# Kernel optimization log

Measured on AMD Instinct MI355X. Metric: run time of the kernel, lower is better.

## Reference

```python
import jax, jax.numpy as jnp
import numpy as np

B, N, M, Wlen = 4, 20000, 64, 8


def setup_inputs() -> dict:
    key = jax.random.key(0)
    k1, k2, k3, k4 = jax.random.split(key, 4)
    a0 = jax.random.uniform(k1, (B, N), dtype=jnp.float32)
    W = 0.01 * jax.random.normal(k2, (M, M), dtype=jnp.float32)
    X1 = jax.random.randint(k3, (M, N, Wlen, 2), 0, N, dtype=jnp.int64)
    X2 = jax.random.randint(k4, (M, N, Wlen, 2), 0, N, dtype=jnp.int64)
    return {"a0": a0, "W": W, "X1": X1, "X2": X2, "T": 2}


def f_clause_stack(a, X):
    # a: [B,n], X: [m,n,w,2] -> [B,m,n]
    y1 = a[:, X[..., 0]]  # [B,m,n,w] gather
    y2 = a[:, X[..., 1]]
    return jnp.max(y1 * y2, axis=3)


def predicate_forward(a, W, X1, X2, temperature=1.0):
    F1 = f_clause_stack(a, X1)  # [B,m1,n]
    F2 = f_clause_stack(a, X2)  # [B,m2,n]
    pi = jax.nn.softmax((W / temperature).reshape(-1)).reshape(W.shape)  # [m1,m2]
    pi1 = pi.sum(axis=1)  # [m1]
    pi2 = pi.sum(axis=0)  # [m2]
    Eu = jnp.einsum('j,bjn->bn', pi1, F1)
    Ev = jnp.einsum('k,bkn->bn', pi2, F2)
    Mt = jnp.einsum('jk,bkn->bjn', pi, F2)
    Euv = jnp.sum(F1 * Mt, axis=1)
    return Eu + Ev - Euv  # [B,n]


def reference(a0, W, X1, X2, T):
    a = a0
    for _ in range(T):  # T is a small static int
        derived = predicate_forward(a, W, X1, X2)
        # single intensional predicate -> stack/max over predicates is identity
        a = 1.0 - (1.0 - a) * (1.0 - derived)
    return a
```

## Files before the change

kernel.cpp:

```cpp
#include <hip/hip_runtime.h>

#define NN 20000

typedef _Float16 f16x2 __attribute__((ext_vector_type(2)));
typedef unsigned short u16x2 __attribute__((ext_vector_type(2)));

union U32H2 { unsigned int u; f16x2 h; };
union U32S2 { unsigned int u; u16x2 s; };

__device__ __forceinline__ f16x2 bc_h2(unsigned int u) { U32H2 x; x.u = u; return x.h; }
__device__ __forceinline__ unsigned int dup_h(float v) {
    _Float16 h = (_Float16)v;
    unsigned short b = __builtin_bit_cast(unsigned short, h);
    return ((unsigned int)b << 16) | b;
}
__device__ __forceinline__ unsigned int pkrtz_u32(float a, float b) {
    return __builtin_bit_cast(unsigned int, __builtin_amdgcn_cvt_pkrtz(a, b));
}
template <int CTRL>
__device__ __forceinline__ unsigned int or_dpp(unsigned int v) {
    return v | (unsigned int)__builtin_amdgcn_update_dpp(0, (int)v, CTRL, 0xF, 0xF, true);
}

__global__ __launch_bounds__(1024) void setup_kernel(const float* __restrict__ W,
                                                     const float* __restrict__ a0,
                                                     unsigned int* __restrict__ pi_t_pk,
                                                     unsigned int* __restrict__ pi1_pk,
                                                     unsigned int* __restrict__ pi2_pk,
                                                     unsigned int* __restrict__ T0) {
    const int t = threadIdx.x;
    if (blockIdx.x != 20) {
        int i = blockIdx.x * 1024 + t;
        if (i < NN) {
            unsigned int b0 = __float2uint_rn(__saturatef(a0[i]) * 255.0f);
            unsigned int b1 = __float2uint_rn(__saturatef(a0[NN + i]) * 255.0f);
            unsigned int b2 = __float2uint_rn(__saturatef(a0[2 * NN + i]) * 255.0f);
            unsigned int b3 = __float2uint_rn(__saturatef(a0[3 * NN + i]) * 255.0f);
            T0[i] = b0 | (b1 << 8) | (b2 << 16) | (b3 << 24);
        }
        return;
    }
    __shared__ float red[1024];
    __shared__ float piL[4096];
    float4 wv = ((const float4*)W)[t];
    float m = fmaxf(fmaxf(wv.x, wv.y), fmaxf(wv.z, wv.w));
    red[t] = m; __syncthreads();
    for (int s = 512; s > 0; s >>= 1) {
        if (t < s) red[t] = fmaxf(red[t], red[t + s]);
        __syncthreads();
    }
    m = red[0];
    __syncthreads();
    float e0 = expf(wv.x - m), e1 = expf(wv.y - m);
    float e2 = expf(wv.z - m), e3 = expf(wv.w - m);
    red[t] = e0 + e1 + e2 + e3;
    __syncthreads();
    for (int s = 512; s > 0; s >>= 1) {
        if (t < s) red[t] += red[t + s];
        __syncthreads();
    }
    float inv = 1.0f / red[0];
    float p[4] = { e0 * inv, e1 * inv, e2 * inv, e3 * inv };
#pragma unroll
    for (int i = 0; i < 4; i++) {
        int f = t * 4 + i;
        piL[f] = p[i];
        pi_t_pk[(f & 63) * 64 + (f >> 6)] = dup_h(p[i]);
    }
    __syncthreads();
    if (t < 64) {
        float s = 0.f;
        for (int k = 0; k < 64; k++) s += piL[t * 64 + k];
        pi1_pk[t] = dup_h(s);
    } else if (t < 128) {
        int k = t - 64;
        float s = 0.f;
        for (int j = 0; j < 64; j++) s += piL[j * 64 + k];
        pi2_pk[k] = dup_h(s);
    }
}

#define ADDRC(nb)                                                    \
    do {                                                             \
        int n_;                                                      \
        n_ = (nb) + n8;      lofA = (n_ < NN ? n_ : NN - 1) * 64;    \
        n_ = (nb) + 8 + n8;  lofB = (n_ < NN ? n_ : NN - 1) * 64;    \
        n_ = (nb) + 16 + n8; lofC = (n_ < NN ? n_ : NN - 1) * 64;    \
        n_ = (nb) + 24 + n8; lofD = (n_ < NN ? n_ : NN - 1) * 64;    \
    } while (0)

#define LDX(x0, x1, x2, x3, lof)                                     \
    do {                                                             \
        x0 = *(const int4*)(Xrow + (lof));                           \
        x1 = *(const int4*)(Xrow + (lof) + 16);                      \
        x2 = *(const int4*)(Xrow + (lof) + 32);                      \
        x3 = *(const int4*)(Xrow + (lof) + 48);                      \
    } while (0)

#define PPAIR(ga, gb)                                                \
    do {                                                             \
        unsigned int ea_ = (ga) & 0x00FF00FFu;                       \
        unsigned int oa_ = __builtin_amdgcn_perm(0u, (ga), 0x0C030C01u); \
        unsigned int eb_ = (gb) & 0x00FF00FFu;                       \
        unsigned int ob_ = __builtin_amdgcn_perm(0u, (gb), 0x0C030C01u); \
        U32S2 pe_, po_, xx_;                                         \
        pe_.u = ea_; xx_.u = eb_; pe_.s = pe_.s * xx_.s;             \
        po_.u = oa_; xx_.u = ob_; po_.s = po_.s * xx_.s;             \
        me.s = __builtin_elementwise_max(me.s, pe_.s);               \
        mo.s = __builtin_elementwise_max(mo.s, po_.s);               \
    } while (0)

#define PH1_OC(db, occ, cn, x0, x1, x2, x3)                          \
    do {                                                             \
        if (8 * (occ) < (cn)) {                                      \
            unsigned int g0 = tab[x0.x], g1 = tab[x0.y];             \
            unsigned int g2 = tab[x0.z], g3 = tab[x0.w];             \
            unsigned int g4 = tab[x1.x], g5 = tab[x1.y];             \
            unsigned int g6 = tab[x1.z], g7 = tab[x1.w];             \
            unsigned int g8 = tab[x2.x], g9 = tab[x2.y];             \
            unsigned int g10 = tab[x2.z], g11 = tab[x2.w];           \
            unsigned int g12 = tab[x3.x], g13 = tab[x3.y];           \
            unsigned int g14 = tab[x3.z], g15 = tab[x3.w];           \
            U32S2 me, mo; me.u = 0u; mo.u = 0u;                      \
            PPAIR(g0, g1);  PPAIR(g2, g3);  PPAIR(g4, g5);  PPAIR(g6, g7); \
            PPAIR(g8, g9);  PPAIR(g10, g11); PPAIR(g12, g13); PPAIR(g14, g15); \
            int col_ = (occ) * 8 + n8;                               \
            if (col_ < (cn)) {                                       \
                float f0_ = (float)(me.u & 0xFFFFu) * sc;            \
                float f1_ = (float)(mo.u & 0xFFFFu) * sc;            \
                float f2_ = (float)(me.u >> 16) * sc;                \
                float f3_ = (float)(mo.u >> 16) * sc;                \
                *(uint2*)&Ft[db][row][col_][0] =                     \
                    make_uint2(pkrtz_u32(f0_, f1_), pkrtz_u32(f2_, f3_)); \
            }                                                        \
        }                                                            \
    } while (0)

template <int ITER>
__global__ __launch_bounds__(1024, 4) void fused_iter(
    const unsigned int* __restrict__ Tsrc,
    const int* __restrict__ X1, const int* __restrict__ X2,
    const unsigned int* __restrict__ pi_t_pk,
    const unsigned int* __restrict__ pi1_pk,
    const unsigned int* __restrict__ pi2_pk,
    const float* __restrict__ a0,
    unsigned int* __restrict__ Tdst, float* __restrict__ outP) {
    __shared__ unsigned int tab[NN];
    __shared__ unsigned int Ft[2][128][30][2];
    __shared__ float redp[2][8][64][4];

    const int t = threadIdx.x;
    const int bid = (int)blockIdx.x;
    const int bstart = bid < 32 ? bid * 79 : 32 * 79 + (bid - 32) * 78;
    const int bcnt = bid < 32 ? 79 : 78;

    const int wid = t >> 6, lane = t & 63;
    const int widu = __builtin_amdgcn_readfirstlane(wid);
    const int r8 = lane >> 3, n8 = lane & 7;
    const int row = widu * 8 + r8;
    const int k = row & 63;
    const int q = t >> 7, bp = (t >> 6) & 1, n_l = t & 63;
    const int qu = __builtin_amdgcn_readfirstlane(q);
    const char* Xrow = (const char*)(widu >= 8 ? X2 : X1)
                     + (size_t)((unsigned)(k * NN)) * 64u;
    const float sc = 1.0f / 65025.0f;

    int lofA, lofB, lofC, lofD;
    int4 xA0, xA1, xA2, xA3, xB0, xB1, xB2, xB3;
    int4 xC0, xC1, xC2, xC3, xD0, xD1, xD2, xD3;

    auto ph2 = [&](int sb, int cn) {
        float part0 = 0.f, part1 = 0.f;
        if (n_l < cn) {
            f16x2 zero = {(_Float16)0, (_Float16)0};
            f16x2 f1v[8];
            f16x2 eu = zero;
#pragma unroll
            for (int jj = 0; jj < 8; ++jj) {
                f1v[jj] = bc_h2(Ft[sb][qu * 8 + jj][n_l][bp]);
                eu += bc_h2(pi1_pk[qu * 8 + jj]) * f1v[jj];
            }
            f16x2 euv = zero, ev = zero;
#pragma unroll 8
            for (int k2 = 0; k2 < 64; ++k2) {
                f16x2 f2 = bc_h2(Ft[sb][64 + k2][n_l][bp]);
                const uint4* pt = (const uint4*)(pi_t_pk + k2 * 64 + qu * 8);
                uint4 w0 = pt[0], w1 = pt[1];
                f16x2 ts = bc_h2(w0.x) * f1v[0] + bc_h2(w0.y) * f1v[1] +
                           bc_h2(w0.z) * f1v[2] + bc_h2(w0.w) * f1v[3] +
                           bc_h2(w1.x) * f1v[4] + bc_h2(w1.y) * f1v[5] +
                           bc_h2(w1.z) * f1v[6] + bc_h2(w1.w) * f1v[7];
                euv += f2 * ts;
                if (qu == 0) ev += bc_h2(pi2_pk[k2]) * f2;
            }
            part0 = (float)eu[0] - (float)euv[0];
            part1 = (float)eu[1] - (float)euv[1];
            if (qu == 0) {
                part0 += (float)ev[0];
                part1 += (float)ev[1];
            }
        }
        *(float2*)&redp[sb][q][n_l][bp * 2] = make_float2(part0, part1);
    };

    auto comb = [&](int pb, int nb, int cn) {
        if (t < 256) {
            int n = t >> 2, b = t & 3;
            if (n < cn) {
                float d = 0.f;
#pragma unroll
                for (int q8 = 0; q8 < 8; ++q8) d += redp[pb][q8][n][b];
                int gn = nb + n;
                float ap;
                if (ITER == 1) ap = a0[(size_t)b * NN + gn];
                else ap = (float)((tab[gn] >> (8 * b)) & 255u) * (1.0f / 255.0f);
                float an = 1.0f - (1.0f - ap) * (1.0f - d);
                if (ITER == 1) {
                    unsigned int v = __float2uint_rn(__saturatef(an) * 255.0f) << (8 * b);
                    v = or_dpp<0xB1>(v);
                    v = or_dpp<0x4E>(v);
                    if (b == 0) Tdst[gn] = v;
                } else {
                    outP[(size_t)b * NN + gn] = an;
                }
            }
        }
    };

    ADDRC(bstart);
    LDX(xA0, xA1, xA2, xA3, lofA);
    LDX(xB0, xB1, xB2, xB3, lofB);
    __builtin_amdgcn_sched_barrier(0);
    for (int i = t; i < NN; i += 1024) tab[i] = Tsrc[i];
    __syncthreads();
    LDX(xC0, xC1, xC2, xC3, lofC);
    LDX(xD0, xD1, xD2, xD3, lofD);
    __builtin_amdgcn_sched_barrier(0);
    PH1_OC(0, 0, 30, xA0, xA1, xA2, xA3);
    PH1_OC(0, 1, 30, xB0, xB1, xB2, xB3);
    PH1_OC(0, 2, 30, xC0, xC1, xC2, xC3);
    PH1_OC(0, 3, 30, xD0, xD1, xD2, xD3);
    __syncthreads();

    for (int r = 0; r < 3; ++r) {
        const int sb = r & 1, db = sb ^ 1;
        if (r < 2) {
            ADDRC(bstart + 30 * (r + 1));
            LDX(xA0, xA1, xA2, xA3, lofA);
            LDX(xB0, xB1, xB2, xB3, lofB);
            __builtin_amdgcn_sched_barrier(0);
        }
        if (r > 0) comb(db, bstart + 30 * (r - 1), 30);
        {
            int cnr = bcnt - 30 * r; cnr = cnr > 30 ? 30 : cnr;
            ph2(sb, cnr);
        }
        if (r < 2) {
            int cn1 = bcnt - 30 * (r + 1); cn1 = cn1 > 30 ? 30 : cn1;
            LDX(xC0, xC1, xC2, xC3, lofC);
            LDX(xD0, xD1, xD2, xD3, lofD);
            __builtin_amdgcn_sched_barrier(0);
            PH1_OC(db, 0, cn1, xA0, xA1, xA2, xA3);
            PH1_OC(db, 1, cn1, xB0, xB1, xB2, xB3);
            PH1_OC(db, 2, cn1, xC0, xC1, xC2, xC3);
            PH1_OC(db, 3, cn1, xD0, xD1, xD2, xD3);
        }
        __syncthreads();
    }
    comb(0, bstart + 60, bcnt - 60);
}

extern "C" void kernel_launch(void* const* d_in, const int* in_sizes, int n_in,
                              void* d_out, int out_size, void* d_ws, size_t ws_size,
                              hipStream_t stream) {
    const float* a0 = (const float*)d_in[0];
    const float* W = (const float*)d_in[1];
    const int* X1 = (const int*)d_in[2];
    const int* X2 = (const int*)d_in[3];
    float* out = (float*)d_out;

    if (ws_size < (size_t)193280) return;
    unsigned int* pi_t   = (unsigned int*)((char*)d_ws + 16384);
    unsigned int* pi1_pk = (unsigned int*)((char*)d_ws + 32768);
    unsigned int* pi2_pk = (unsigned int*)((char*)d_ws + 33024);
    unsigned int* T0     = (unsigned int*)((char*)d_ws + 33280);
    unsigned int* T1     = (unsigned int*)((char*)d_ws + 113280);

    setup_kernel<<<21, 1024, 0, stream>>>(W, a0, pi_t, pi1_pk, pi2_pk, T0);
    fused_iter<1><<<256, 1024, 0, stream>>>(T0, X1, X2, pi_t, pi1_pk, pi2_pk,
                                            a0, T1, nullptr);
    fused_iter<2><<<256, 1024, 0, stream>>>(T1, X1, X2, pi_t, pi1_pk, pi2_pk,
                                            nullptr, nullptr, out);
}
```

Baseline: 248.6 us.

## Split batch into two pairs per block with half-size blocks and 16-bit tables

Each block now handles two of the four batch entries, with 512 threads per block and twice as many blocks. The gather table shrinks to 16-bit entries, halving LDS use per block so more blocks can fit per CU. The phase-1 index loads become a rolling prefetch of one quad ahead over 16 rows per wave. The trade-off is that every X index is now read twice across the grid, once per batch pair, which doubles global index traffic.

```diff
diff --git a/kernel.cpp b/kernel.cpp
--- a/kernel.cpp
+++ b/kernel.cpp
@@ -1,6 +1,7 @@
 #include <hip/hip_runtime.h>
 
 #define NN 20000
+#define POFF (8 * NN * 64)
 
 typedef _Float16 f16x2 __attribute__((ext_vector_type(2)));
 typedef unsigned short u16x2 __attribute__((ext_vector_type(2)));
@@ -17,9 +18,8 @@
 __device__ __forceinline__ unsigned int pkrtz_u32(float a, float b) {
     return __builtin_bit_cast(unsigned int, __builtin_amdgcn_cvt_pkrtz(a, b));
 }
-template <int CTRL>
-__device__ __forceinline__ unsigned int or_dpp(unsigned int v) {
-    return v | (unsigned int)__builtin_amdgcn_update_dpp(0, (int)v, CTRL, 0xF, 0xF, true);
+__device__ __forceinline__ unsigned int or_dpp_x1(unsigned int v) {
+    return v | (unsigned int)__builtin_amdgcn_update_dpp(0, (int)v, 0xB1, 0xF, 0xF, true);
 }
 
 __global__ __launch_bounds__(1024) void setup_kernel(const float* __restrict__ W,
@@ -27,7 +27,7 @@
                                                      unsigned int* __restrict__ pi_t_pk,
                                                      unsigned int* __restrict__ pi1_pk,
                                                      unsigned int* __restrict__ pi2_pk,
-                                                     unsigned int* __restrict__ T0) {
+                                                     unsigned short* __restrict__ T0) {
     const int t = threadIdx.x;
     if (blockIdx.x != 20) {
         int i = blockIdx.x * 1024 + t;
@@ -36,7 +36,8 @@
             unsigned int b1 = __float2uint_rn(__saturatef(a0[NN + i]) * 255.0f);
             unsigned int b2 = __float2uint_rn(__saturatef(a0[2 * NN + i]) * 255.0f);
             unsigned int b3 = __float2uint_rn(__saturatef(a0[3 * NN + i]) * 255.0f);
-            T0[i] = b0 | (b1 << 8) | (b2 << 16) | (b3 << 24);
+            T0[i] = (unsigned short)(b0 | (b1 << 8));
+            T0[NN + i] = (unsigned short)(b2 | (b3 << 8));
         }
         return;
     }
@@ -80,94 +81,99 @@
     }
 }
 
-#define ADDRC(nb)                                                    \
-    do {                                                             \
-        int n_;                                                      \
-        n_ = (nb) + n8;      lofA = (n_ < NN ? n_ : NN - 1) * 64;    \
-        n_ = (nb) + 8 + n8;  lofB = (n_ < NN ? n_ : NN - 1) * 64;    \
-        n_ = (nb) + 16 + n8; lofC = (n_ < NN ? n_ : NN - 1) * 64;    \
-        n_ = (nb) + 24 + n8; lofD = (n_ < NN ? n_ : NN - 1) * 64;    \
-    } while (0)
-
-#define LDX(x0, x1, x2, x3, lof)                                     \
-    do {                                                             \
-        x0 = *(const int4*)(Xrow + (lof));                           \
-        x1 = *(const int4*)(Xrow + (lof) + 16);                      \
-        x2 = *(const int4*)(Xrow + (lof) + 32);                      \
-        x3 = *(const int4*)(Xrow + (lof) + 48);                      \
-    } while (0)
-
-#define PPAIR(ga, gb)                                                \
-    do {                                                             \
-        unsigned int ea_ = (ga) & 0x00FF00FFu;                       \
-        unsigned int oa_ = __builtin_amdgcn_perm(0u, (ga), 0x0C030C01u); \
-        unsigned int eb_ = (gb) & 0x00FF00FFu;                       \
-        unsigned int ob_ = __builtin_amdgcn_perm(0u, (gb), 0x0C030C01u); \
-        U32S2 pe_, po_, xx_;                                         \
-        pe_.u = ea_; xx_.u = eb_; pe_.s = pe_.s * xx_.s;             \
-        po_.u = oa_; xx_.u = ob_; po_.s = po_.s * xx_.s;             \
-        me.s = __builtin_elementwise_max(me.s, pe_.s);               \
-        mo.s = __builtin_elementwise_max(mo.s, po_.s);               \
-    } while (0)
-
-#define PH1_OC(db, occ, cn, x0, x1, x2, x3)                          \
-    do {                                                             \
-        if (8 * (occ) < (cn)) {                                      \
-            unsigned int g0 = tab[x0.x], g1 = tab[x0.y];             \
-            unsigned int g2 = tab[x0.z], g3 = tab[x0.w];             \
-            unsigned int g4 = tab[x1.x], g5 = tab[x1.y];             \
-            unsigned int g6 = tab[x1.z], g7 = tab[x1.w];             \
-            unsigned int g8 = tab[x2.x], g9 = tab[x2.y];             \
-            unsigned int g10 = tab[x2.z], g11 = tab[x2.w];           \
-            unsigned int g12 = tab[x3.x], g13 = tab[x3.y];           \
-            unsigned int g14 = tab[x3.z], g15 = tab[x3.w];           \
-            U32S2 me, mo; me.u = 0u; mo.u = 0u;                      \
-            PPAIR(g0, g1);  PPAIR(g2, g3);  PPAIR(g4, g5);  PPAIR(g6, g7); \
-            PPAIR(g8, g9);  PPAIR(g10, g11); PPAIR(g12, g13); PPAIR(g14, g15); \
-            int col_ = (occ) * 8 + n8;                               \
-            if (col_ < (cn)) {                                       \
-                float f0_ = (float)(me.u & 0xFFFFu) * sc;            \
-                float f1_ = (float)(mo.u & 0xFFFFu) * sc;            \
-                float f2_ = (float)(me.u >> 16) * sc;                \
-                float f3_ = (float)(mo.u >> 16) * sc;                \
-                *(uint2*)&Ft[db][row][col_][0] =                     \
-                    make_uint2(pkrtz_u32(f0_, f1_), pkrtz_u32(f2_, f3_)); \
-            }                                                        \
-        }                                                            \
+#define ADDRC(nb)                                                     \
+    do {                                                              \
+        int n_;                                                       \
+        n_ = (nb) + n8;      lofA = rb64 + (n_ < NN ? n_ : NN - 1) * 64; \
+        n_ = (nb) + 8 + n8;  lofB = rb64 + (n_ < NN ? n_ : NN - 1) * 64; \
+        n_ = (nb) + 16 + n8; lofC = rb64 + (n_ < NN ? n_ : NN - 1) * 64; \
+        n_ = (nb) + 24 + n8; lofD = rb64 + (n_ < NN ? n_ : NN - 1) * 64; \
+    } while (0)
+
+#define LDXQ(x0, x1, x2, x3, off)                                     \
+    do {                                                              \
+        x0 = *(const int4*)(Xrow + (off));                            \
+        x1 = *(const int4*)(Xrow + (off) + 16);                       \
+        x2 = *(const int4*)(Xrow + (off) + 32);                       \
+        x3 = *(const int4*)(Xrow + (off) + 48);                       \
+    } while (0)
+
+#define GPAIR(ia, ib)                                                 \
+    do {                                                              \
+        unsigned int gx_ = (unsigned int)tab[ia];                     \
+        unsigned int gy_ = (unsigned int)tab[ib];                     \
+        unsigned int A_ = __builtin_amdgcn_perm(0u, gx_, 0x0C010C00u); \
+        unsigned int B_ = __builtin_amdgcn_perm(0u, gy_, 0x0C010C00u); \
+        U32S2 pa_, pb_; pa_.u = A_; pb_.u = B_;                       \
+        pa_.s = pa_.s * pb_.s;                   \
+        mx.s = __builtin_elementwise_max(mx.s, pa_.s);                \
+    } while (0)
+
+#define PH1STEP(db, occ, pss, cn, x0, x1, x2, x3)                     \
+    do {                                                              \
+        if (8 * (occ) < (cn)) {                                       \
+            U32S2 mx; mx.u = 0u;                                      \
+            GPAIR(x0.x, x0.y); GPAIR(x0.z, x0.w);                     \
+            GPAIR(x1.x, x1.y); GPAIR(x1.z, x1.w);                     \
+            GPAIR(x2.x, x2.y); GPAIR(x2.z, x2.w);                     \
+            GPAIR(x3.x, x3.y); GPAIR(x3.z, x3.w);                     \
+            int col_ = (occ) * 8 + n8;                                \
+            if (col_ < (cn)) {                                        \
+                float f0_ = (float)(mx.u & 0xFFFFu) * sc;             \
+                float f1_ = (float)(mx.u >> 16) * sc;                 \
+                Ft[db][row0 + (pss) * 8][col_] = pkrtz_u32(f0_, f1_); \
+            }                                                         \
+        }                                                             \
+    } while (0)
+
+#define CPX do { cx0 = nx0; cx1 = nx1; cx2 = nx2; cx3 = nx3; } while (0)
+
+#define PH1CHUNK(db, cn)                                              \
+    do {                                                              \
+        LDXQ(nx0, nx1, nx2, nx3, lofA + POFF); PH1STEP(db, 0, 0, cn, cx0, cx1, cx2, cx3); CPX; \
+        LDXQ(nx0, nx1, nx2, nx3, lofB);        PH1STEP(db, 0, 1, cn, cx0, cx1, cx2, cx3); CPX; \
+        LDXQ(nx0, nx1, nx2, nx3, lofB + POFF); PH1STEP(db, 1, 0, cn, cx0, cx1, cx2, cx3); CPX; \
+        LDXQ(nx0, nx1, nx2, nx3, lofC);        PH1STEP(db, 1, 1, cn, cx0, cx1, cx2, cx3); CPX; \
+        LDXQ(nx0, nx1, nx2, nx3, lofC + POFF); PH1STEP(db, 2, 0, cn, cx0, cx1, cx2, cx3); CPX; \
+        LDXQ(nx0, nx1, nx2, nx3, lofD);        PH1STEP(db, 2, 1, cn, cx0, cx1, cx2, cx3); CPX; \
+        LDXQ(nx0, nx1, nx2, nx3, lofD + POFF); PH1STEP(db, 3, 0, cn, cx0, cx1, cx2, cx3); CPX; \
+        PH1STEP(db, 3, 1, cn, cx0, cx1, cx2, cx3);                    \
     } while (0)
 
 template <int ITER>
-__global__ __launch_bounds__(1024, 4) void fused_iter(
-    const unsigned int* __restrict__ Tsrc,
+__global__ __launch_bounds__(512, 4) void fused_iter(
+    const unsigned short* __restrict__ Tsrc,
     const int* __restrict__ X1, const int* __restrict__ X2,
     const unsigned int* __restrict__ pi_t_pk,
     const unsigned int* __restrict__ pi1_pk,
     const unsigned int* __restrict__ pi2_pk,
     const float* __restrict__ a0,
-    unsigned int* __restrict__ Tdst, float* __restrict__ outP) {
-    __shared__ unsigned int tab[NN];
-    __shared__ unsigned int Ft[2][128][30][2];
-    __shared__ float redp[2][8][64][4];
+    unsigned short* __restrict__ Tdst, float* __restrict__ outP) {
+    __shared__ unsigned short tab[NN];
+    __shared__ unsigned int Ft[2][128][30];
+    __shared__ float redp[2][8][64][2];
 
     const int t = threadIdx.x;
     const int bid = (int)blockIdx.x;
-    const int bstart = bid < 32 ? bid * 79 : 32 * 79 + (bid - 32) * 78;
-    const int bcnt = bid < 32 ? 79 : 78;
+    const int rng = bid & 255;
+    const int pair = bid >> 8;
+    const int bstart = rng < 32 ? rng * 79 : 32 * 79 + (rng - 32) * 78;
+    const int bcnt = rng < 32 ? 79 : 78;
 
     const int wid = t >> 6, lane = t & 63;
     const int widu = __builtin_amdgcn_readfirstlane(wid);
     const int r8 = lane >> 3, n8 = lane & 7;
-    const int row = widu * 8 + r8;
-    const int k = row & 63;
-    const int q = t >> 7, bp = (t >> 6) & 1, n_l = t & 63;
-    const int qu = __builtin_amdgcn_readfirstlane(q);
-    const char* Xrow = (const char*)(widu >= 8 ? X2 : X1)
-                     + (size_t)((unsigned)(k * NN)) * 64u;
+    const int row0 = widu * 16 + r8;
+    const int n_l = t & 63;
+    const int qu = widu;
+    const char* Xrow = (const char*)(widu >= 4 ? X2 : X1)
+                     + (size_t)((widu & 3) * 16) * (size_t)(NN * 64);
+    const int rb64 = r8 * NN * 64;
     const float sc = 1.0f / 65025.0f;
+    const unsigned short* Tp = Tsrc + (size_t)pair * NN;
 
     int lofA, lofB, lofC, lofD;
-    int4 xA0, xA1, xA2, xA3, xB0, xB1, xB2, xB3;
-    int4 xC0, xC1, xC2, xC3, xD0, xD1, xD2, xD3;
+    int4 cx0, cx1, cx2, cx3, nx0, nx1, nx2, nx3;
 
     auto ph2 = [&](int sb, int cn) {
         float part0 = 0.f, part1 = 0.f;
@@ -177,13 +183,13 @@
             f16x2 eu = zero;
 #pragma unroll
             for (int jj = 0; jj < 8; ++jj) {
-                f1v[jj] = bc_h2(Ft[sb][qu * 8 + jj][n_l][bp]);
+                f1v[jj] = bc_h2(Ft[sb][qu * 8 + jj][n_l]);
                 eu += bc_h2(pi1_pk[qu * 8 + jj]) * f1v[jj];
             }
             f16x2 euv = zero, ev = zero;
 #pragma unroll 8
             for (int k2 = 0; k2 < 64; ++k2) {
-                f16x2 f2 = bc_h2(Ft[sb][64 + k2][n_l][bp]);
+                f16x2 f2 = bc_h2(Ft[sb][64 + k2][n_l]);
                 const uint4* pt = (const uint4*)(pi_t_pk + k2 * 64 + qu * 8);
                 uint4 w0 = pt[0], w1 = pt[1];
                 f16x2 ts = bc_h2(w0.x) * f1v[0] + bc_h2(w0.y) * f1v[1] +
@@ -200,54 +206,46 @@
                 part1 += (float)ev[1];
             }
         }
-        *(float2*)&redp[sb][q][n_l][bp * 2] = make_float2(part0, part1);
+        *(float2*)&redp[sb][qu][n_l][0] = make_float2(part0, part1);
     };
 
     auto comb = [&](int pb, int nb, int cn) {
-        if (t < 256) {
-            int n = t >> 2, b = t & 3;
+        if (t < 128) {
+            int n = t >> 1, b = t & 1;
             if (n < cn) {
                 float d = 0.f;
 #pragma unroll
                 for (int q8 = 0; q8 < 8; ++q8) d += redp[pb][q8][n][b];
                 int gn = nb + n;
                 float ap;
-                if (ITER == 1) ap = a0[(size_t)b * NN + gn];
+                if (ITER == 1) ap = a0[(size_t)(pair * 2 + b) * NN + gn];
                 else ap = (float)((tab[gn] >> (8 * b)) & 255u) * (1.0f / 255.0f);
                 float an = 1.0f - (1.0f - ap) * (1.0f - d);
                 if (ITER == 1) {
                     unsigned int v = __float2uint_rn(__saturatef(an) * 255.0f) << (8 * b);
-                    v = or_dpp<0xB1>(v);
-                    v = or_dpp<0x4E>(v);
-                    if (b == 0) Tdst[gn] = v;
+                    v = or_dpp_x1(v);
+                    if (b == 0) Tdst[(size_t)pair * NN + gn] = (unsigned short)v;
                 } else {
-                    outP[(size_t)b * NN + gn] = an;
+                    outP[(size_t)(pair * 2 + b) * NN + gn] = an;
                 }
             }
         }
     };
 
     ADDRC(bstart);
-    LDX(xA0, xA1, xA2, xA3, lofA);
-    LDX(xB0, xB1, xB2, xB3, lofB);
+    LDXQ(cx0, cx1, cx2, cx3, lofA);
     __builtin_amdgcn_sched_barrier(0);
-    for (int i = t; i < NN; i += 1024) tab[i] = Tsrc[i];
-    __syncthreads();
-    LDX(xC0, xC1, xC2, xC3, lofC);
-    LDX(xD0, xD1, xD2, xD3, lofD);
-    __builtin_amdgcn_sched_barrier(0);
-    PH1_OC(0, 0, 30, xA0, xA1, xA2, xA3);
-    PH1_OC(0, 1, 30, xB0, xB1, xB2, xB3);
-    PH1_OC(0, 2, 30, xC0, xC1, xC2, xC3);
-    PH1_OC(0, 3, 30, xD0, xD1, xD2, xD3);
+    for (int i = t; i < (NN / 2); i += 512)
+        ((unsigned int*)tab)[i] = ((const unsigned int*)Tp)[i];
+    __syncthreads();
+    PH1CHUNK(0, 30);
     __syncthreads();
 
     for (int r = 0; r < 3; ++r) {
         const int sb = r & 1, db = sb ^ 1;
         if (r < 2) {
             ADDRC(bstart + 30 * (r + 1));
-            LDX(xA0, xA1, xA2, xA3, lofA);
-            LDX(xB0, xB1, xB2, xB3, lofB);
+            LDXQ(cx0, cx1, cx2, cx3, lofA);
             __builtin_amdgcn_sched_barrier(0);
         }
         if (r > 0) comb(db, bstart + 30 * (r - 1), 30);
@@ -257,13 +255,7 @@
         }
         if (r < 2) {
             int cn1 = bcnt - 30 * (r + 1); cn1 = cn1 > 30 ? 30 : cn1;
-            LDX(xC0, xC1, xC2, xC3, lofC);
-            LDX(xD0, xD1, xD2, xD3, lofD);
-            __builtin_amdgcn_sched_barrier(0);
-            PH1_OC(db, 0, cn1, xA0, xA1, xA2, xA3);
-            PH1_OC(db, 1, cn1, xB0, xB1, xB2, xB3);
-            PH1_OC(db, 2, cn1, xC0, xC1, xC2, xC3);
-            PH1_OC(db, 3, cn1, xD0, xD1, xD2, xD3);
+            PH1CHUNK(db, cn1);
         }
         __syncthreads();
     }
@@ -280,15 +272,15 @@
     float* out = (float*)d_out;
 
     if (ws_size < (size_t)193280) return;
-    unsigned int* pi_t   = (unsigned int*)((char*)d_ws + 16384);
-    unsigned int* pi1_pk = (unsigned int*)((char*)d_ws + 32768);
-    unsigned int* pi2_pk = (unsigned int*)((char*)d_ws + 33024);
-    unsigned int* T0     = (unsigned int*)((char*)d_ws + 33280);
-    unsigned int* T1     = (unsigned int*)((char*)d_ws + 113280);
+    unsigned int* pi_t    = (unsigned int*)((char*)d_ws + 16384);
+    unsigned int* pi1_pk  = (unsigned int*)((char*)d_ws + 32768);
+    unsigned int* pi2_pk  = (unsigned int*)((char*)d_ws + 33024);
+    unsigned short* T0    = (unsigned short*)((char*)d_ws + 33280);
+    unsigned short* T1    = (unsigned short*)((char*)d_ws + 113280);
 
     setup_kernel<<<21, 1024, 0, stream>>>(W, a0, pi_t, pi1_pk, pi2_pk, T0);
-    fused_iter<1><<<256, 1024, 0, stream>>>(T0, X1, X2, pi_t, pi1_pk, pi2_pk,
-                                            a0, T1, nullptr);
-    fused_iter<2><<<256, 1024, 0, stream>>>(T1, X1, X2, pi_t, pi1_pk, pi2_pk,
-                                            nullptr, nullptr, out);
-}
+    fused_iter<1><<<512, 512, 0, stream>>>(T0, X1, X2, pi_t, pi1_pk, pi2_pk,
+                                           a0, T1, nullptr);
+    fused_iter<2><<<512, 512, 0, stream>>>(T1, X1, X2, pi_t, pi1_pk, pi2_pk,
+                                           nullptr, nullptr, out);
+}
```

Result: slower. 285.5 us (+14.8%).
